# Kernel tuning notes

Measured on AMD Instinct MI355X. Metric: run time of the kernel, lower is better.

## Reference

```python
import jax, jax.numpy as jnp
import numpy as np

B, S, D, E, NH, R, L = 512, 23, 768, 8, 8, 256, 50
TOP_K = 2
LN_EPS = 1e-5  # torch LayerNorm default


def _ln(x, g, b):
    m = jnp.mean(x, axis=-1, keepdims=True)
    v = jnp.mean((x - m) ** 2, axis=-1, keepdims=True)
    return (x - m) * jax.lax.rsqrt(v + LN_EPS) * g + b


def setup_inputs() -> dict:
    key = jax.random.key(0)
    it = iter(jax.random.split(key, 32))
    def p(shape, scale=0.02):
        return jax.random.normal(next(it), shape, dtype=jnp.float32) * scale
    inp = {
        'section_embeddings': jax.random.normal(next(it), (B, S, D), dtype=jnp.float32),
        'existing': jax.random.randint(next(it), (B, S), 0, 2, dtype=jnp.int32),
        'missing_table': p((S, D), 0.05),
        # DeepPositionEncoder per expert (num_layers=3): D->R->R->R->D + LN(D)
        'dpe_w0': p((E, D, R)), 'dpe_b0': jnp.zeros((E, R), jnp.float32),
        'dpe_w1': p((E, R, R)), 'dpe_b1': jnp.zeros((E, R), jnp.float32),
        'dpe_w2': p((E, R, R)), 'dpe_b2': jnp.zeros((E, R), jnp.float32),
        'dpe_wo': p((E, R, D)), 'dpe_bo': jnp.zeros((E, D), jnp.float32),
        'dpe_ln_g': jnp.ones((E, D), jnp.float32), 'dpe_ln_b': jnp.zeros((E, D), jnp.float32),
        # fusion_mlp: cat([context,pos]) (2D)->R->D ; W1 split into context/pos halves
        'fus_w1c': p((E, D, R)), 'fus_w1p': p((E, D, R)), 'fus_b1': jnp.zeros((E, R), jnp.float32),
        'fus_w2': p((E, R, D)), 'fus_b2': jnp.zeros((E, D), jnp.float32),
        # gate_mlp: 2D->R->1, sigmoid
        'gate_w1c': p((E, D, R)), 'gate_w1p': p((E, D, R)), 'gate_b1': jnp.zeros((E, R), jnp.float32),
        'gate_w2': p((E, R, 1)), 'gate_b2': jnp.zeros((E, 1), jnp.float32),
        'exp_ln_g': jnp.ones((E, D), jnp.float32), 'exp_ln_b': jnp.zeros((E, D), jnp.float32),
        # router: 2D->R->E
        'rtr_w1': p((2 * D, R)), 'rtr_b1': jnp.zeros((R,), jnp.float32),
        'rtr_w2': p((R, E)), 'rtr_b2': jnp.zeros((E,), jnp.float32),
        # SectionDimReducer: D->D//2->R + LN(R)
        'red_w1': p((D, D // 2)), 'red_b1': jnp.zeros((D // 2,), jnp.float32),
        'red_w2': p((D // 2, R)), 'red_b2': jnp.zeros((R,), jnp.float32),
        'red_ln_g': jnp.ones((R,), jnp.float32), 'red_ln_b': jnp.zeros((R,), jnp.float32),
        # MultiheadAttention (embed_dim=R, heads=NH)
        'qkv_w': p((3, R, R)), 'qkv_b': jnp.zeros((3, R), jnp.float32),
        'out_w': p((R, R)), 'out_b': jnp.zeros((R,), jnp.float32),
        # predictor
        'pred_w': p((R, L)), 'pred_b': jnp.zeros((L,), jnp.float32),
    }
    return inp


def reference(section_embeddings, existing, missing_table,
              dpe_w0, dpe_b0, dpe_w1, dpe_b1, dpe_w2, dpe_b2, dpe_wo, dpe_bo,
              dpe_ln_g, dpe_ln_b,
              fus_w1c, fus_w1p, fus_b1, fus_w2, fus_b2,
              gate_w1c, gate_w1p, gate_b1, gate_w2, gate_b2,
              exp_ln_g, exp_ln_b,
              rtr_w1, rtr_b1, rtr_w2, rtr_b2,
              red_w1, red_b1, red_w2, red_b2, red_ln_g, red_ln_b,
              qkv_w, qkv_b, out_w, out_b, pred_w, pred_b):
    mask = existing.astype(section_embeddings.dtype)[..., None]         # [B,S,1]
    # masked mean context over present sections
    context = (section_embeddings * mask).sum(1) / (mask.sum(1) + 1e-8)  # [B,D]
    T = B * S
    default = jnp.broadcast_to(missing_table[None], (B, S, D)).reshape(T, D)
    ctx = jnp.broadcast_to(context[:, None, :], (B, S, D)).reshape(T, D)
    # --- all experts, dense (as in source) ---
    h = jax.nn.relu(jnp.einsum('td,edh->teh', default, dpe_w0) + dpe_b0)
    h = jax.nn.relu(jnp.einsum('teh,ehk->tek', h, dpe_w1) + dpe_b1)
    h = jax.nn.relu(jnp.einsum('teh,ehk->tek', h, dpe_w2) + dpe_b2)
    pos = _ln(jnp.einsum('teh,ehd->ted', h, dpe_wo) + dpe_bo + default[:, None, :],
              dpe_ln_g, dpe_ln_b)                                        # [T,E,D]
    hf = jax.nn.relu(jnp.einsum('td,edh->teh', ctx, fus_w1c)
                     + jnp.einsum('ted,edh->teh', pos, fus_w1p) + fus_b1)
    cand = jnp.einsum('teh,ehd->ted', hf, fus_w2) + fus_b2
    hg = jax.nn.relu(jnp.einsum('td,edh->teh', ctx, gate_w1c)
                     + jnp.einsum('ted,edh->teh', pos, gate_w1p) + gate_b1)
    gate = jax.nn.sigmoid(jnp.einsum('teh,eho->teo', hg, gate_w2) + gate_b2)  # [T,E,1]
    exp_out = _ln(gate * cand + (1.0 - gate) * ctx[:, None, :], exp_ln_g, exp_ln_b)  # [T,E,D]
    # --- router: softmax -> top-k -> sparse scatter ---
    rin = jnp.concatenate([default, ctx], axis=-1)                      # [T,2D]
    scores = jax.nn.relu(rin @ rtr_w1 + rtr_b1) @ rtr_w2 + rtr_b2       # [T,E]
    w = jax.nn.softmax(scores, axis=-1)
    tv, ti = jax.lax.top_k(w, TOP_K)
    sw = jnp.zeros_like(w).at[jnp.arange(T)[:, None], ti].set(tv)       # [T,E]
    imputed = jnp.einsum('ted,te->td', exp_out, sw).reshape(B, S, D)
    sec = mask * section_embeddings + (1.0 - mask) * imputed            # [B,S,D]
    # --- reducer ---
    x = jax.nn.gelu(sec @ red_w1 + red_b1, approximate=False)
    x = jax.nn.gelu(x @ red_w2 + red_b2, approximate=False)
    x = _ln(x, red_ln_g, red_ln_b)                                      # [B,S,R]
    # --- MHA self-attention over sections ---
    hd = R // NH
    q = (x @ qkv_w[0] + qkv_b[0]).reshape(B, S, NH, hd)
    k = (x @ qkv_w[1] + qkv_b[1]).reshape(B, S, NH, hd)
    v = (x @ qkv_w[2] + qkv_b[2]).reshape(B, S, NH, hd)
    att = jax.nn.softmax(jnp.einsum('bqhd,bkhd->bhqk', q, k) / np.sqrt(hd), axis=-1)
    o = jnp.einsum('bhqk,bkhd->bqhd', att, v).reshape(B, S, R)
    o = o @ out_w + out_b
    logits = o.mean(axis=1) @ pred_w + pred_b                           # [B,L]
    return logits
```

## Files before the change

### kernel.cpp

```cpp
#include <hip/hip_runtime.h>
#include <hip/hip_bf16.h>
#include <math.h>

#define BB  512
#define SS  23
#define DD  768
#define EE  8
#define NHH 8
#define RR  256
#define HDD 32
#define LL  50
#define HH2 384
#define TT  (BB*SS)
#define LN_EPS 1e-5f
#define MAXWORK 1536
#define NCTX 4352
#define NACAP 12288
#define CPAD 64

typedef short v8s __attribute__((ext_vector_type(8)));
typedef float v4f __attribute__((ext_vector_type(4)));

__device__ __forceinline__ float gelu(float v){
  return 0.5f*v*(1.f + erff(v*0.70710678118654752f));
}
__device__ __forceinline__ unsigned short f2b(float v){
  __hip_bfloat16 h = __float2bfloat16(v);
  return *reinterpret_cast<unsigned short*>(&h);
}

__device__ __forceinline__ float block_sum(float v, float* red, int nw){
  #pragma unroll
  for (int o = 32; o > 0; o >>= 1) v += __shfl_down(v, o, 64);
  int wid = threadIdx.x >> 6;
  __syncthreads();
  if ((threadIdx.x & 63) == 0) red[wid] = v;
  __syncthreads();
  float s = 0.f;
  for (int i = 0; i < nw; ++i) s += red[i];
  return s;
}

__global__ void k_context(const float* __restrict__ emb, const int* __restrict__ existing,
                          float* __restrict__ ctx, unsigned short* __restrict__ ctxbf){
  int b = blockIdx.x, tid = threadIdx.x;
  float acc0=0.f, acc1=0.f, acc2=0.f;
  int cnt = 0;
  for (int s = 0; s < SS; ++s){
    if (existing[b*SS + s]){
      ++cnt;
      const float* row = emb + ((size_t)(b*SS + s))*DD;
      acc0 += row[tid]; acc1 += row[tid+256]; acc2 += row[tid+512];
    }
  }
  float inv = 1.0f / ((float)cnt + 1e-8f);
  float v0 = acc0*inv, v1 = acc1*inv, v2 = acc2*inv;
  ctx[(size_t)b*DD + tid      ] = v0;
  ctx[(size_t)b*DD + tid + 256] = v1;
  ctx[(size_t)b*DD + tid + 512] = v2;
  ctxbf[(size_t)b*DD + tid      ] = f2b(v0);
  ctxbf[(size_t)b*DD + tid + 256] = f2b(v1);
  ctxbf[(size_t)b*DD + tid + 512] = f2b(v2);
}

__global__ void k_mtpad(const float* __restrict__ mt, unsigned short* __restrict__ mtbf){
  int row = blockIdx.x, tid = threadIdx.x;
  #pragma unroll
  for (int j = 0; j < 3; ++j){
    int d = tid + j*256;
    float v = (row < SS) ? mt[(size_t)row*DD + d] : 0.f;
    mtbf[(size_t)row*DD + d] = f2b(v);
  }
}

__global__ __launch_bounds__(256) void k_pack(
    const float* __restrict__ red_w1, const float* __restrict__ qkv_w,
    const float* __restrict__ out_w,  const float* __restrict__ fus_w1c,
    const float* __restrict__ gate_w1c, const float* __restrict__ fus_w2,
    const float* __restrict__ rtr_w1,
    const float* __restrict__ dpe_w0, const float* __restrict__ dpe_w1,
    const float* __restrict__ dpe_w2, const float* __restrict__ dpe_wo,
    const float* __restrict__ fus_w1p, const float* __restrict__ gate_w1p,
    const float* __restrict__ red_w2,
    unsigned short* __restrict__ Wr1t, unsigned short* __restrict__ Wqt,
    unsigned short* __restrict__ Wot,  unsigned short* __restrict__ Wct,
    unsigned short* __restrict__ Wf2t,
    unsigned short* __restrict__ W0t,  unsigned short* __restrict__ W1t,
    unsigned short* __restrict__ W2t,  unsigned short* __restrict__ Wot2,
    unsigned short* __restrict__ Wpgt, unsigned short* __restrict__ Wr1rt,
    unsigned short* __restrict__ Wr2t){
  int t = blockIdx.x, tid = threadIdx.x;
  const float* src; unsigned short* dst;
  int Nsrc, stride, tk, tn;
  if (t < 288){ src = red_w1; dst = Wr1t; Nsrc = 384; stride = 768; tk = t % 24; tn = t / 24; }
  else if (t < 480){
    int u = t - 288, m = u >> 6, v2 = u & 63;
    src = qkv_w + (size_t)m*256*256; dst = Wqt + (size_t)m*256*256;
    Nsrc = 256; stride = 256; tk = v2 & 7; tn = v2 >> 3;
  } else if (t < 544){
    int v2 = t - 480;
    src = out_w; dst = Wot; Nsrc = 256; stride = 256; tk = v2 & 7; tn = v2 >> 3;
  } else if (t < 2080){
    int u = t - 544, e = u / 192, v2 = u % 192;
    src = fus_w1c + (size_t)e*DD*RR; dst = Wct + (size_t)(e*256)*768;
    Nsrc = 256; stride = 768; tk = v2 % 24; tn = v2 / 24;
  } else if (t < 3616){
    int u = t - 2080, e = u / 192, v2 = u % 192;
    src = gate_w1c + (size_t)e*DD*RR; dst = Wct + (size_t)(2048 + e*256)*768;
    Nsrc = 256; stride = 768; tk = v2 % 24; tn = v2 / 24;
  } else if (t < 5152){
    int u = t - 3616, e = u / 192, v2 = u % 192;
    src = fus_w2 + (size_t)e*RR*DD; dst = Wf2t + (size_t)e*768*256;
    Nsrc = 768; stride = 256; tk = v2 & 7; tn = v2 >> 3;
  } else if (t < 5344){
    int u = t - 5152;
    src = rtr_w1 + (size_t)768*256; dst = Wct + (size_t)4096*768;
    Nsrc = 256; stride = 768; tk = u % 24; tn = u / 24;
  } else if (t < 6880){
    int u = t - 5344, e = u / 192, v2 = u % 192;
    src = dpe_w0 + (size_t)e*DD*RR; dst = W0t + (size_t)e*256*768;
    Nsrc = 256; stride = 768; tk = v2 % 24; tn = v2 / 24;
  } else if (t < 7392){
    int u = t - 6880, e = u / 64, v2 = u % 64;
    src = dpe_w1 + (size_t)e*RR*RR; dst = W1t + (size_t)e*256*256;
    Nsrc = 256; stride = 256; tk = v2 & 7; tn = v2 >> 3;
  } else if (t < 7904){
    int u = t - 7392, e = u / 64, v2 = u % 64;
    src = dpe_w2 + (size_t)e*RR*RR; dst = W2t + (size_t)e*256*256;
    Nsrc = 256; stride = 256; tk = v2 & 7; tn = v2 >> 3;
  } else if (t < 9440){
    int u = t - 7904, e = u / 192, v2 = u % 192;
    src = dpe_wo + (size_t)e*RR*DD; dst = Wot2 + (size_t)e*768*256;
    Nsrc = 768; stride = 256; tk = v2 & 7; tn = v2 >> 3;
  } else if (t < 10976){
    int u = t - 9440, e = u / 192, v2 = u % 192;
    src = fus_w1p + (size_t)e*DD*RR; dst = Wpgt + (size_t)e*512*768;
    Nsrc = 256; stride = 768; tk = v2 % 24; tn = v2 / 24;
  } else if (t < 12512){
    int u = t - 10976, e = u / 192, v2 = u % 192;
    src = gate_w1p + (size_t)e*DD*RR; dst = Wpgt + (size_t)e*512*768 + (size_t)256*768;
    Nsrc = 256; stride = 768; tk = v2 % 24; tn = v2 / 24;
  } else if (t < 12704){
    int u = t - 12512;
    src = rtr_w1; dst = Wr1rt;
    Nsrc = 256; stride = 768; tk = u % 24; tn = u / 24;
  } else {
    int u = t - 12704;
    src = red_w2; dst = Wr2t;
    Nsrc = 256; stride = 384; tk = u % 12; tn = u / 12;
  }
  __shared__ float lt[32][33];
  int i0 = tid >> 5, j = tid & 31;
  #pragma unroll
  for (int l = 0; l < 4; ++l){
    int i = i0 + l*8;
    lt[i][j] = src[(size_t)(tk*32 + i)*Nsrc + tn*32 + j];
  }
  __syncthreads();
  #pragma unroll
  for (int l = 0; l < 4; ++l){
    int i = i0 + l*8;
    dst[(size_t)(tn*32 + i)*stride + tk*32 + j] = f2b(lt[j][i]);
  }
}

__global__ __launch_bounds__(256) void k_gemm(
    const unsigned short* __restrict__ A, const unsigned short* __restrict__ Bt,
    const float* __restrict__ bias, float* __restrict__ C,
    int M, int N, int K, int epi){
  int m0 = blockIdx.x * 64, n0 = blockIdx.y * 64;
  int tid = threadIdx.x;
  int w = tid >> 6, lane = tid & 63;
  int fm = lane & 15, q = lane >> 4;
  __shared__ unsigned short As[64*72];
  __shared__ unsigned short Bs[64*72];
  v4f acc[4] = {};
  int sr = tid >> 2, scb = (tid & 3) * 16;
  const unsigned short* Aga = A + (size_t)(m0 + sr)*K + scb;
  const unsigned short* Bga = Bt + (size_t)(n0 + sr)*K + scb;
  unsigned short* Asd = As + sr*72 + scb;
  unsigned short* Bsd = Bs + sr*72 + scb;
  for (int k0 = 0; k0 < K; k0 += 64){
    uint4 a0 = *(const uint4*)(Aga + k0);
    uint4 a1 = *(const uint4*)(Aga + k0 + 8);
    uint4 b0 = *(const uint4*)(Bga + k0);
    uint4 b1 = *(const uint4*)(Bga + k0 + 8);
    __syncthreads();
    *(uint4*)Asd = a0; *(uint4*)(Asd + 8) = a1;
    *(uint4*)Bsd = b0; *(uint4*)(Bsd + 8) = b1;
    __syncthreads();
    const unsigned short* ap = As + (w*16 + fm)*72 + q*8;
    const unsigned short* bp = Bs + fm*72 + q*8;
    #pragma unroll
    for (int kk = 0; kk < 2; ++kk){
      v8s af = *(const v8s*)(ap + kk*32);
      #pragma unroll
      for (int j = 0; j < 4; ++j){
        v8s bf = *(const v8s*)(bp + j*16*72 + kk*32);
        acc[j] = __builtin_amdgcn_mfma_f32_16x16x32_bf16(af, bf, acc[j], 0, 0, 0);
      }
    }
  }
  #pragma unroll
  for (int j = 0; j < 4; ++j){
    int n = n0 + j*16 + fm;
    float bv = bias ? bias[n] : 0.f;
    if (epi == 3){
      unsigned short* Cp = (unsigned short*)C + (size_t)(m0 + w*16 + q*4)*N + n;
      #pragma unroll
      for (int r = 0; r < 4; ++r)
        Cp[(size_t)r*N] = f2b(gelu(acc[j][r] + bv));
    } else {
      float* Cp = C + (size_t)(m0 + w*16 + q*4)*N + n;
      #pragma unroll
      for (int r = 0; r < 4; ++r){
        float v = acc[j][r] + bv;
        if (epi == 2) v = gelu(v);
        Cp[(size_t)r*N] = v;
      }
    }
  }
}

__global__ __launch_bounds__(256) void k_gemmb(
    const unsigned short* __restrict__ A, size_t sA,
    const unsigned short* __restrict__ Bt, size_t sB,
    const float* __restrict__ bias, int sbias,
    void* __restrict__ C, size_t sC,
    int M, int N, int K, int epi){
  int e = blockIdx.z;
  const unsigned short* Ae = A + (size_t)e*sA;
  const unsigned short* Be = Bt + (size_t)e*sB;
  const float* biase = bias ? (bias + (size_t)e*sbias) : (const float*)nullptr;
  int m0 = blockIdx.x * 64, n0 = blockIdx.y * 64;
  int tid = threadIdx.x;
  int w = tid >> 6, lane = tid & 63;
  int fm = lane & 15, q = lane >> 4;
  __shared__ unsigned short As[64*72];
  __shared__ unsigned short Bs[64*72];
  v4f acc[4] = {};
  int sr = tid >> 2, scb = (tid & 3) * 16;
  const unsigned short* Aga = Ae + (size_t)(m0 + sr)*K + scb;
  const unsigned short* Bga = Be + (size_t)(n0 + sr)*K + scb;
  unsigned short* Asd = As + sr*72 + scb;
  unsigned short* Bsd = Bs + sr*72 + scb;
  for (int k0 = 0; k0 < K; k0 += 64){
    uint4 a0 = *(const uint4*)(Aga + k0);
    uint4 a1 = *(const uint4*)(Aga + k0 + 8);
    uint4 b0 = *(const uint4*)(Bga + k0);
    uint4 b1 = *(const uint4*)(Bga + k0 + 8);
    __syncthreads();
    *(uint4*)Asd = a0; *(uint4*)(Asd + 8) = a1;
    *(uint4*)Bsd = b0; *(uint4*)(Bsd + 8) = b1;
    __syncthreads();
    const unsigned short* ap = As + (w*16 + fm)*72 + q*8;
    const unsigned short* bp = Bs + fm*72 + q*8;
    #pragma unroll
    for (int kk = 0; kk < 2; ++kk){
      v8s af = *(const v8s*)(ap + kk*32);
      #pragma unroll
      for (int j = 0; j < 4; ++j){
        v8s bf = *(const v8s*)(bp + j*16*72 + kk*32);
        acc[j] = __builtin_amdgcn_mfma_f32_16x16x32_bf16(af, bf, acc[j], 0, 0, 0);
      }
    }
  }
  #pragma unroll
  for (int j = 0; j < 4; ++j){
    int n = n0 + j*16 + fm;
    float bv = biase ? biase[n] : 0.f;
    #pragma unroll
    for (int r = 0; r < 4; ++r){
      float v = acc[j][r] + bv;
      int m = m0 + w*16 + q*4 + r;
      if (epi == 0){
        unsigned short* Cb = (unsigned short*)C + (size_t)e*sC;
        Cb[(size_t)m*N + n] = f2b(fmaxf(v, 0.f));
      } else {
        float* Cf = (float*)C + (size_t)e*sC;
        Cf[(size_t)m*N + n] = v;
      }
    }
  }
}

__global__ void k_posLN(const float* __restrict__ dpeout, const float* __restrict__ mt,
                        const float* __restrict__ lng, const float* __restrict__ lnb,
                        unsigned short* __restrict__ posbf){
  int e = blockIdx.x >> 6, s = blockIdx.x & 63, tid = threadIdx.x;
  size_t ro = (size_t)(e*64 + s)*DD;
  if (s >= SS){
    for (int j = tid; j < DD; j += 256) posbf[ro + j] = 0;
    return;
  }
  __shared__ float red[8];
  float o[3];
  #pragma unroll
  for (int j = 0; j < 3; ++j){
    int d = tid + j*256;
    o[j] = dpeout[ro + d] + mt[(size_t)s*DD + d];
  }
  float mean = block_sum(o[0]+o[1]+o[2], red, 4) * (1.f/DD);
  float dv = 0.f;
  #pragma unroll
  for (int j = 0; j < 3; ++j){ float c = o[j]-mean; dv += c*c; }
  float rstd = rsqrtf(block_sum(dv, red, 4) * (1.f/DD) + LN_EPS);
  #pragma unroll
  for (int j = 0; j < 3; ++j){
    int d = tid + j*256;
    posbf[ro + d] = f2b((o[j]-mean)*rstd*lng[e*DD + d] + lnb[e*DD + d]);
  }
}

__global__ __launch_bounds__(256) void k_router(
    const float* __restrict__ emb, const int* __restrict__ existing,
    const float* __restrict__ rtrD, const float* __restrict__ ctxFGR,
    const float* __restrict__ rb1, const float* __restrict__ rw2,
    const float* __restrict__ rb2,
    int* __restrict__ cntE, int* __restrict__ listE,
    int* __restrict__ bp0, int* __restrict__ bp1, float* __restrict__ w01,
    unsigned short* __restrict__ secbf){
  int wv = threadIdx.x >> 6, lane = threadIdx.x & 63;
  int tid = threadIdx.x;
  int t = blockIdx.x*4 + wv;
  __shared__ int   easc[8];
  __shared__ int   slotA[8];
  int ex = existing[t];
  if (ex){
    const float4* src = (const float4*)(emb + (size_t)t*DD);
    uint2* dst = (uint2*)(secbf + (size_t)t*DD);
    #pragma unroll
    for (int j = 0; j < 3; ++j){
      float4 x = src[lane + j*64];
      uint2 pk;
      pk.x = (unsigned)f2b(x.x) | ((unsigned)f2b(x.y) << 16);
      pk.y = (unsigned)f2b(x.z) | ((unsigned)f2b(x.w) << 16);
      dst[lane + j*64] = pk;
    }
    if (lane == 0){ easc[2*wv] = -1; easc[2*wv+1] = -1; }
  } else {
    int b = t / SS, s = t - b*SS;
    const float* rtrC = ctxFGR + (size_t)b*NCTX + 4096;
    float acc[EE] = {};
    #pragma unroll
    for (int j = 0; j < 4; ++j){
      int idx = lane + j*64;
      float hr = fmaxf(rtrD[s*RR + idx] + rtrC[idx] + rb1[idx], 0.f);
      #pragma unroll
      for (int e = 0; e < EE; ++e) acc[e] += hr * rw2[idx*EE + e];
    }
    #pragma unroll
    for (int e = 0; e < EE; ++e)
      #pragma unroll
      for (int o = 32; o > 0; o >>= 1) acc[e] += __shfl_xor(acc[e], o, 64);
    if (lane == 0){
      float sc[EE];
      float m = -1e30f;
      #pragma unroll
      for (int e = 0; e < EE; ++e){ sc[e] = acc[e] + rb2[e]; m = fmaxf(m, sc[e]); }
      float w[EE]; float Z = 0.f;
      #pragma unroll
      for (int e = 0; e < EE; ++e){ w[e] = expf(sc[e]-m); Z += w[e]; }
      int i0 = 0;
      for (int e = 1; e < EE; ++e) if (w[e] > w[i0]) i0 = e;
      int i1 = -1;
      for (int e = 0; e < EE; ++e) if (e != i0 && (i1 < 0 || w[e] > w[i1])) i1 = e;
      float iz = 1.f/Z;
      easc[2*wv]   = i0; w01[2*t]   = w[i0]*iz;
      easc[2*wv+1] = i1; w01[2*t+1] = w[i1]*iz;
    }
  }
  __syncthreads();
  if (tid < EE){
    int e = tid, c = 0;
    #pragma unroll
    for (int j = 0; j < 8; ++j) if (easc[j] == e) ++c;
    if (c){
      int base = atomicAdd(&cntE[e*CPAD], c);
      int sl = base;
      #pragma unroll
      for (int j = 0; j < 8; ++j) if (easc[j] == e) slotA[j] = sl++;
    }
  }
  __syncthreads();
  if (tid < 8){
    int j = tid, e = easc[j];
    if (e >= 0){
      int tt = blockIdx.x*4 + (j >> 1);
      int sl = slotA[j];
      if (sl >= TT) sl = TT - 1;
      listE[e*TT + sl] = tt;
      int bp = (e << 16) | sl;
      if (j & 1) bp1[tt] = bp;
      else       bp0[tt] = bp;
    }
  }
}

__global__ void k_offsE(const int* __restrict__ cntE, int* __restrict__ offE,
                        int* __restrict__ workE, int* __restrict__ wtotE){
  if (threadIdx.x == 0){
    int acc = 0, wb = 0;
    for (int e = 0; e < EE; ++e){
      offE[e] = acc;
      int n = cntE[e*CPAD]; if (n > TT) n = TT;
      acc += n;
      int nb = (n + 63) >> 6;
      for (int j = 0; j < nb && wb < MAXWORK; ++j) workE[wb++] = (e << 16) | j;
    }
    wtotE[0] = wb;
  }
}

__global__ __launch_bounds__(256) void k_hfE(
    const float* __restrict__ ctxFGR, const float* __restrict__ posFG,
    const float* __restrict__ fb1,
    const float* __restrict__ gb1, const float* __restrict__ gw2,
    const float* __restrict__ gb2,
    const int* __restrict__ cntE, const int* __restrict__ offE,
    const int* __restrict__ listE,
    const int* __restrict__ workE, const int* __restrict__ wtotE,
    unsigned short* __restrict__ hfg, float* __restrict__ gatesg){
  int wi = blockIdx.x;
  if (wi >= wtotE[0]) return;
  int ent = workE[wi];
  int e = ent >> 16, chunk = ent & 0xffff;
  int n = cntE[e*CPAD]; if (n > TT) n = TT;
  int nt = n - chunk*64; if (nt > 64) nt = 64;
  int base = offE[e] + chunk*64;
  int tid = threadIdx.x, wv = tid >> 6, lane = tid & 63;
  __shared__ int tb[64], ts[64];
  if (tid < 64){
    int ok = tid < nt;
    int t = listE[e*TT + chunk*64 + (ok ? tid : 0)];
    tb[tid] = t/SS; ts[tid] = t - (t/SS)*SS;
  }
  __syncthreads();
  {
    int row = tid >> 2, cb = (tid & 3) * 64;
    if (row < nt){
      int b = tb[row], s = ts[row];
      const float4* cF = (const float4*)(ctxFGR + (size_t)b*NCTX + e*256 + cb);
      const float4* pF = (const float4*)(posFG + ((size_t)(e*64 + s))*512 + cb);
      const float4* bF = (const float4*)(fb1 + (size_t)e*RR + cb);
      uint2* dst = (uint2*)(hfg + (size_t)(base + row)*256 + cb);
      #pragma unroll
      for (int j = 0; j < 16; ++j){
        float4 a = cF[j], p = pF[j], bb = bF[j];
        uint2 pk;
        pk.x = (unsigned)f2b(fmaxf(a.x+p.x+bb.x, 0.f))
             | ((unsigned)f2b(fmaxf(a.y+p.y+bb.y, 0.f)) << 16);
        pk.y = (unsigned)f2b(fmaxf(a.z+p.z+bb.z, 0.f))
             | ((unsigned)f2b(fmaxf(a.w+p.w+bb.w, 0.f)) << 16);
        dst[j] = pk;
      }
    }
  }
  for (int ii = 0; ii < 16; ++ii){
    int row = wv*16 + ii;
    if (row < nt){
      int b = tb[row], s = ts[row];
      float g = 0.f;
      #pragma unroll
      for (int j = 0; j < 4; ++j){
        int idx = lane + j*64;
        float hg = fmaxf(ctxFGR[(size_t)b*NCTX + 2048 + e*256 + idx]
                         + posFG[((size_t)(e*64 + s))*512 + 256 + idx] + gb1[e*RR + idx], 0.f);
        g += hg * gw2[e*RR + idx];
      }
      #pragma unroll
      for (int o = 32; o > 0; o >>= 1) g += __shfl_xor(g, o, 64);
      if (lane == 0) gatesg[base + row] = 1.f/(1.f + expf(-(g + gb2[e])));
    }
  }
}

__global__ __launch_bounds__(256) void k_gemmE(
    const unsigned short* __restrict__ hfg, const unsigned short* __restrict__ Wf2t,
    const float* __restrict__ fb2, const float* __restrict__ ctx,
    const float* __restrict__ gatesg,
    const int* __restrict__ cntE, const int* __restrict__ offE,
    const int* __restrict__ listE,
    const int* __restrict__ workE, const int* __restrict__ wtotE,
    float* __restrict__ cand){
  int wi = blockIdx.x;
  if (wi >= wtotE[0]) return;
  int ent = workE[wi];
  int e = ent >> 16, chunk = ent & 0xffff;
  int n = cntE[e*CPAD]; if (n > TT) n = TT;
  int nt = n - chunk*64; if (nt > 64) nt = 64;
  int base = offE[e] + chunk*64;
  int nc = blockIdx.y;
  int tid = threadIdx.x, w = tid >> 6, lane = tid & 63;
  int fm = lane & 15, q = lane >> 4;
  __shared__ unsigned short As[64*72];
  __shared__ unsigned short Bs[64*72];
  __shared__ float gl[64];
  __shared__ int tbl[64];
  if (tid < 64){
    int ok = tid < nt;
    int t = listE[e*TT + chunk*64 + (ok ? tid : 0)];
    tbl[tid] = t/SS;
    gl[tid] = gatesg[base + (ok ? tid : 0)];
  }
  v4f acc[4] = {};
  int sr = tid >> 2, scb = (tid & 3) * 16;
  const unsigned short* Aga = hfg + (size_t)(base + sr)*256 + scb;
  const unsigned short* Bga = Wf2t + (size_t)e*768*256 + (size_t)(nc*64 + sr)*256 + scb;
  unsigned short* Asd = As + sr*72 + scb;
  unsigned short* Bsd = Bs + sr*72 + scb;
  for (int k0 = 0; k0 < 256; k0 += 64){
    uint4 a0 = *(const uint4*)(Aga + k0);
    uint4 a1 = *(const uint4*)(Aga + k0 + 8);
    uint4 b0 = *(const uint4*)(Bga + k0);
    uint4 b1 = *(const uint4*)(Bga + k0 + 8);
    __syncthreads();
    *(uint4*)Asd = a0; *(uint4*)(Asd + 8) = a1;
    *(uint4*)Bsd = b0; *(uint4*)(Bsd + 8) = b1;
    __syncthreads();
    const unsigned short* ap = As + (w*16 + fm)*72 + q*8;
    const unsigned short* bp = Bs + fm*72 + q*8;
    #pragma unroll
    for (int kk = 0; kk < 2; ++kk){
      v8s af = *(const v8s*)(ap + kk*32);
      #pragma unroll
      for (int j = 0; j < 4; ++j){
        v8s bf = *(const v8s*)(bp + j*16*72 + kk*32);
        acc[j] = __builtin_amdgcn_mfma_f32_16x16x32_bf16(af, bf, acc[j], 0, 0, 0);
      }
    }
  }
  #pragma unroll
  for (int j = 0; j < 4; ++j){
    int d = nc*64 + j*16 + fm;
    float fb2v = fb2[(size_t)e*DD + d];
    #pragma unroll
    for (int r = 0; r < 4; ++r){
      int row = w*16 + q*4 + r;
      if (row < nt){
        float g = gl[row];
        float cv = ctx[(size_t)tbl[row]*DD + d];
        cand[(size_t)(base + row)*DD + d] = g*(acc[j][r] + fb2v) + (1.f - g)*cv;
      }
    }
  }
}

__global__ void k_gather(const int* __restrict__ existing,
                         const int* __restrict__ bp0, const int* __restrict__ bp1,
                         const float* __restrict__ w01, const int* __restrict__ offE,
                         const float* __restrict__ cand,
                         const float* __restrict__ elng, const float* __restrict__ elnb,
                         unsigned short* __restrict__ secbf){
  int wv = threadIdx.x >> 6, lane = threadIdx.x & 63;
  int t = blockIdx.x*4 + wv;
  if (existing[t]) return;
  int b0v = bp0[t], b1v = bp1[t];
  int e0 = b0v >> 16, e1 = b1v >> 16;
  int g0 = offE[e0] + (b0v & 0xffff);
  int g1 = offE[e1] + (b1v & 0xffff);
  if (g0 >= NACAP) g0 = 0;
  if (g1 >= NACAP) g1 = 0;
  float w0 = w01[2*t], w1 = w01[2*t+1];
  float v0[12], v1[12];
  float s0 = 0.f, q0 = 0.f, s1 = 0.f, q1 = 0.f;
  #pragma unroll
  for (int j = 0; j < 12; ++j){
    int d = lane + j*64;
    v0[j] = cand[(size_t)g0*DD + d];
    v1[j] = cand[(size_t)g1*DD + d];
    s0 += v0[j]; q0 += v0[j]*v0[j];
    s1 += v1[j]; q1 += v1[j]*v1[j];
  }
  #pragma unroll
  for (int o = 32; o > 0; o >>= 1){
    s0 += __shfl_xor(s0, o, 64); q0 += __shfl_xor(q0, o, 64);
    s1 += __shfl_xor(s1, o, 64); q1 += __shfl_xor(q1, o, 64);
  }
  float mean0 = s0*(1.f/DD), mean1 = s1*(1.f/DD);
  float rstd0 = rsqrtf(q0*(1.f/DD) - mean0*mean0 + LN_EPS);
  float rstd1 = rsqrtf(q1*(1.f/DD) - mean1*mean1 + LN_EPS);
  #pragma unroll
  for (int j = 0; j < 12; ++j){
    int d = lane + j*64;
    float o0 = (v0[j]-mean0)*rstd0*elng[e0*DD + d] + elnb[e0*DD + d];
    float o1 = (v1[j]-mean1)*rstd1*elng[e1*DD + d] + elnb[e1*DD + d];
    secbf[(size_t)t*DD + d] = f2b(w0*o0 + w1*o1);
  }
}

__global__ void k_lnR(const float* __restrict__ x2f,
                      const float* __restrict__ lng, const float* __restrict__ lnb,
                      unsigned short* __restrict__ xrbf){
  int wv = threadIdx.x >> 6, lane = threadIdx.x & 63;
  int t = blockIdx.x*4 + wv;
  float v[4];
  float s = 0.f, q = 0.f;
  #pragma unroll
  for (int j = 0; j < 4; ++j){
    v[j] = x2f[(size_t)t*RR + lane + j*64];
    s += v[j]; q += v[j]*v[j];
  }
  #pragma unroll
  for (int o = 32; o > 0; o >>= 1){
    s += __shfl_xor(s, o, 64); q += __shfl_xor(q, o, 64);
  }
  float mean = s*(1.f/RR);
  float rstd = rsqrtf(q*(1.f/RR) - mean*mean + LN_EPS);
  #pragma unroll
  for (int j = 0; j < 4; ++j){
    int d = lane + j*64;
    xrbf[(size_t)t*RR + d] = f2b((v[j]-mean)*rstd*lng[d] + lnb[d]);
  }
}

__global__ void k_attn(const float* __restrict__ qcat, unsigned short* __restrict__ attnbf){
  int bh = blockIdx.x, b = bh / NHH, h = bh % NHH, tid = threadIdx.x;
  __shared__ float qs[SS][HDD], ks[SS][HDD], vs[SS][HDD];
  __shared__ float scr[SS][SS+1];
  for (int idx = tid; idx < SS*HDD; idx += 256){
    int s = idx / HDD, d = idx % HDD;
    size_t g = ((size_t)(b*SS + s))*768 + h*HDD + d;
    qs[s][d] = qcat[g]; ks[s][d] = qcat[g + 256]; vs[s][d] = qcat[g + 512];
  }
  __syncthreads();
  const float scale = 0.17677669529663687f;
  for (int idx = tid; idx < SS*SS; idx += 256){
    int qi = idx / SS, ki = idx % SS;
    float a = 0.f;
    #pragma unroll
    for (int d = 0; d < HDD; ++d) a += qs[qi][d]*ks[ki][d];
    scr[qi][ki] = a*scale;
  }
  __syncthreads();
  if (tid < SS){
    float m = -1e30f;
    for (int ki = 0; ki < SS; ++ki) m = fmaxf(m, scr[tid][ki]);
    float Z = 0.f;
    for (int ki = 0; ki < SS; ++ki){ float e2 = expf(scr[tid][ki]-m); scr[tid][ki] = e2; Z += e2; }
    float iz = 1.f/Z;
    for (int ki = 0; ki < SS; ++ki) scr[tid][ki] *= iz;
  }
  __syncthreads();
  for (int idx = tid; idx < SS*HDD; idx += 256){
    int qi = idx / HDD, d = idx % HDD;
    float a = 0.f;
    for (int ki = 0; ki < SS; ++ki) a += scr[qi][ki]*vs[ki][d];
    attnbf[((size_t)(b*SS + qi))*RR + h*HDD + d] = f2b(a);
  }
}

__global__ void k_final(const float* __restrict__ oproj, const float* __restrict__ pw,
                        const float* __restrict__ pb, float* __restrict__ out){
  int b = blockIdx.x, tid = threadIdx.x;
  __shared__ float om[RR];
  float a = 0.f;
  for (int s = 0; s < SS; ++s) a += oproj[((size_t)(b*SS + s))*RR + tid];
  om[tid] = a * (1.f/SS);
  __syncthreads();
  if (tid < LL){
    float acc = pb[tid];
    for (int h = 0; h < RR; ++h) acc += om[h]*pw[h*LL + tid];
    out[b*LL + tid] = acc;
  }
}

extern "C" void kernel_launch(void* const* d_in, const int* in_sizes, int n_in,
                              void* d_out, int out_size, void* d_ws, size_t ws_size,
                              hipStream_t stream){
  (void)in_sizes; (void)n_in; (void)out_size; (void)ws_size;
  const float* emb      = (const float*)d_in[0];
  const int*   existing = (const int*)d_in[1];
  const float* mt       = (const float*)d_in[2];
  const float* dpe_w0   = (const float*)d_in[3];
  const float* dpe_b0   = (const float*)d_in[4];
  const float* dpe_w1   = (const float*)d_in[5];
  const float* dpe_b1   = (const float*)d_in[6];
  const float* dpe_w2   = (const float*)d_in[7];
  const float* dpe_b2   = (const float*)d_in[8];
  const float* dpe_wo   = (const float*)d_in[9];
  const float* dpe_bo   = (const float*)d_in[10];
  const float* dpe_lng  = (const float*)d_in[11];
  const float* dpe_lnb  = (const float*)d_in[12];
  const float* fus_w1c  = (const float*)d_in[13];
  const float* fus_w1p  = (const float*)d_in[14];
  const float* fus_b1   = (const float*)d_in[15];
  const float* fus_w2   = (const float*)d_in[16];
  const float* fus_b2   = (const float*)d_in[17];
  const float* gate_w1c = (const float*)d_in[18];
  const float* gate_w1p = (const float*)d_in[19];
  const float* gate_b1  = (const float*)d_in[20];
  const float* gate_w2  = (const float*)d_in[21];
  const float* gate_b2  = (const float*)d_in[22];
  const float* exp_lng  = (const float*)d_in[23];
  const float* exp_lnb  = (const float*)d_in[24];
  const float* rtr_w1   = (const float*)d_in[25];
  const float* rtr_b1   = (const float*)d_in[26];
  const float* rtr_w2   = (const float*)d_in[27];
  const float* rtr_b2   = (const float*)d_in[28];
  const float* red_w1   = (const float*)d_in[29];
  const float* red_b1   = (const float*)d_in[30];
  const float* red_w2   = (const float*)d_in[31];
  const float* red_b2   = (const float*)d_in[32];
  const float* red_lng  = (const float*)d_in[33];
  const float* red_lnb  = (const float*)d_in[34];
  const float* qkv_w    = (const float*)d_in[35];
  const float* qkv_b    = (const float*)d_in[36];
  const float* out_w    = (const float*)d_in[37];
  const float* out_b    = (const float*)d_in[38];
  const float* pred_w   = (const float*)d_in[39];
  const float* pred_b   = (const float*)d_in[40];
  float* out = (float*)d_out;

  float* wsf = (float*)d_ws;
  size_t off = 0;
  float* ctx    = wsf + off; off += (size_t)BB*DD;
  unsigned short* ctxbf = (unsigned short*)(wsf + off); off += (size_t)BB*DD/2;
  float* ctxFGR = wsf + off; off += (size_t)BB*NCTX;
  int*   cntE   = (int*)(wsf + off); off += EE*CPAD;
  int*   workE  = (int*)(wsf + off); off += MAXWORK;
  int*   wtot   = (int*)(wsf + off); off += 64;
  int*   offE   = wtot + 8;
  float* regA   = wsf + off; off += (size_t)128*TT;
  int*   listE  = (int*)regA;
  int*   bp0    = (int*)regA + (size_t)EE*TT;
  int*   bp1    = (int*)regA + (size_t)(EE+1)*TT;
  float* w01    = regA + (size_t)(EE+2)*TT;
  unsigned short* attnbf = (unsigned short*)regA;
  float* regB   = wsf + off; off += (size_t)TT*DD/2;
  unsigned short* secbf = (unsigned short*)regB;
  float* oprojf = regB;
  float* regC   = wsf + off; off += (size_t)NACAP*DD;
  float* dpeout = regC;
  unsigned short* posbf = (unsigned short*)(regC + 393216);
  unsigned short* h0    = (unsigned short*)(regC + 589824);
  unsigned short* h1    = (unsigned short*)(regC + 655360);
  unsigned short* h2    = (unsigned short*)(regC + 720896);
  float* cand   = regC;
  unsigned short* x1bf = (unsigned short*)regC;
  float* x2f    = regC + 4718592;
  float* qcat   = regC;
  float* regD   = wsf + off; off += (size_t)NACAP*256/2;
  unsigned short* hfg  = (unsigned short*)regD;
  unsigned short* xrbf = (unsigned short*)regD;
  unsigned short* Wr1t = (unsigned short*)(wsf + off); off += (size_t)768*384/2;
  unsigned short* Wqt  = (unsigned short*)(wsf + off); off += (size_t)768*256/2;
  unsigned short* Wot  = (unsigned short*)(wsf + off); off += (size_t)256*256/2;
  unsigned short* Wct  = (unsigned short*)(wsf + off); off += (size_t)NCTX*768/2;
  unsigned short* Wf2t = (unsigned short*)(wsf + off); off += (size_t)EE*768*256/2;
  unsigned short* mtbf = (unsigned short*)(wsf + off); off += (size_t)64*768/2;
  unsigned short* W0t  = (unsigned short*)(wsf + off); off += (size_t)EE*256*768/2;
  unsigned short* W1t  = (unsigned short*)(wsf + off); off += (size_t)EE*256*256/2;
  unsigned short* W2t  = (unsigned short*)(wsf + off); off += (size_t)EE*256*256/2;
  unsigned short* Wot2 = (unsigned short*)(wsf + off); off += (size_t)EE*768*256/2;
  unsigned short* Wpgt = (unsigned short*)(wsf + off); off += (size_t)EE*512*768/2;
  unsigned short* Wr1rt= (unsigned short*)(wsf + off); off += (size_t)256*768/2;
  unsigned short* Wr2t = (unsigned short*)(wsf + off); off += (size_t)256*384/2;
  float* posFG  = wsf + off; off += (size_t)EE*64*512;
  float* rtrDp  = wsf + off; off += (size_t)64*256;
  float* gatesg = wsf + off; off += (size_t)NACAP;

  k_context<<<BB, 256, 0, stream>>>(emb, existing, ctx, ctxbf);
  k_mtpad  <<<64, 256, 0, stream>>>(mt, mtbf);
  k_pack   <<<12800, 256, 0, stream>>>(red_w1, qkv_w, out_w, fus_w1c, gate_w1c, fus_w2,
                                       rtr_w1, dpe_w0, dpe_w1, dpe_w2, dpe_wo,
                                       fus_w1p, gate_w1p, red_w2,
                                       Wr1t, Wqt, Wot, Wct, Wf2t,
                                       W0t, W1t, W2t, Wot2, Wpgt, Wr1rt, Wr2t);
  k_gemmb<<<dim3(1,4,8),  256, 0, stream>>>(mtbf, 0, W0t, (size_t)256*768,
                                            dpe_b0, 256, h0, (size_t)64*256,
                                            64, 256, 768, 0);
  k_gemmb<<<dim3(1,4,8),  256, 0, stream>>>(h0, (size_t)64*256, W1t, (size_t)256*256,
                                            dpe_b1, 256, h1, (size_t)64*256,
                                            64, 256, 256, 0);
  k_gemmb<<<dim3(1,4,8),  256, 0, stream>>>(h1, (size_t)64*256, W2t, (size_t)256*256,
                                            dpe_b2, 256, h2, (size_t)64*256,
                                            64, 256, 256, 0);
  k_gemmb<<<dim3(1,12,8), 256, 0, stream>>>(h2, (size_t)64*256, Wot2, (size_t)768*256,
                                            dpe_bo, 768, dpeout, (size_t)64*768,
                                            64, 768, 256, 1);
  k_posLN<<<512, 256, 0, stream>>>(dpeout, mt, dpe_lng, dpe_lnb, posbf);
  k_gemmb<<<dim3(1,8,8),  256, 0, stream>>>(posbf, (size_t)64*768, Wpgt, (size_t)512*768,
                                            (const float*)nullptr, 0, posFG, (size_t)64*512,
                                            64, 512, 768, 1);
  k_gemmb<<<dim3(1,4,1),  256, 0, stream>>>(mtbf, 0, Wr1rt, 0,
                                            (const float*)nullptr, 0, rtrDp, 0,
                                            64, 256, 768, 1);
  {
    dim3 g(BB/64, NCTX/64);
    k_gemm <<<g, 256, 0, stream>>>(ctxbf, Wct, (const float*)nullptr, ctxFGR,
                                   BB, NCTX, DD, 0);
  }
  hipMemsetAsync(cntE, 0, EE*CPAD*sizeof(int), stream);
  k_router <<<TT/4, 256, 0, stream>>>(emb, existing, rtrDp, ctxFGR, rtr_b1, rtr_w2, rtr_b2,
                                      cntE, listE, bp0, bp1, w01, secbf);
  k_offsE  <<<1, 64, 0, stream>>>(cntE, offE, workE, wtot);
  k_hfE    <<<384, 256, 0, stream>>>(ctxFGR, posFG, fus_b1,
                                     gate_b1, gate_w2, gate_b2,
                                     cntE, offE, listE, workE, wtot, hfg, gatesg);
  k_gemmE  <<<dim3(384,12), 256, 0, stream>>>(hfg, Wf2t, fus_b2, ctx, gatesg,
                                              cntE, offE, listE, workE, wtot, cand);
  k_gather <<<TT/4, 256, 0, stream>>>(existing, bp0, bp1, w01, offE, cand,
                                      exp_lng, exp_lnb, secbf);
  {
    dim3 g(TT/64, HH2/64);
    k_gemm <<<g, 256, 0, stream>>>(secbf, Wr1t, red_b1, (float*)x1bf, TT, HH2, DD, 3);
  }
  {
    dim3 g(TT/64, RR/64);
    k_gemm <<<g, 256, 0, stream>>>(x1bf, Wr2t, red_b2, x2f, TT, RR, HH2, 2);
  }
  k_lnR    <<<TT/4, 256, 0, stream>>>(x2f, red_lng, red_lnb, xrbf);
  {
    dim3 g(TT/64, 768/64);
    k_gemm <<<g, 256, 0, stream>>>(xrbf, Wqt, qkv_b, qcat, TT, 768, RR, 1);
  }
  k_attn   <<<BB*NHH, 256, 0, stream>>>(qcat, attnbf);
  {
    dim3 g(TT/64, RR/64);
    k_gemm <<<g, 256, 0, stream>>>(attnbf, Wot, out_b, oprojf, TT, RR, RR, 1);
  }
  k_final  <<<BB, 256, 0, stream>>>(oprojf, pred_w, pred_b, out);
}
```

Before: 464.6 us.

## Fuse reducer second GEMM with LayerNorm, store expert candidates in bf16, merge setup kernels

Replaces the second reducer GEMM plus separate LayerNorm kernel with one kernel that computes a full 256-wide row tile, applies GELU, and normalizes in registers, avoiding the fp32 x2f round trip. Expert candidate outputs are written as bf16 instead of fp32, halving that intermediate's traffic at some precision cost. The missing-table conversion and the expert counter reset are folded into the context kernel, removing a launch and a memset. The fused GEMM uses only TT/64 blocks with a large shared tile and 16 accumulators, which reduces parallelism and may lower occupancy.

```diff
diff --git a/kernel.cpp b/kernel.cpp
--- a/kernel.cpp
+++ b/kernel.cpp
@@ -28,6 +28,10 @@
   __hip_bfloat16 h = __float2bfloat16(v);
   return *reinterpret_cast<unsigned short*>(&h);
 }
+__device__ __forceinline__ float b2f(unsigned short u){
+  unsigned int x = ((unsigned)u) << 16;
+  return __uint_as_float(x);
+}
 
 __device__ __forceinline__ float block_sum(float v, float* red, int nw){
   #pragma unroll
@@ -42,8 +46,19 @@
 }
 
 __global__ void k_context(const float* __restrict__ emb, const int* __restrict__ existing,
-                          float* __restrict__ ctx, unsigned short* __restrict__ ctxbf){
+                          const float* __restrict__ mt,
+                          float* __restrict__ ctx, unsigned short* __restrict__ ctxbf,
+                          unsigned short* __restrict__ mtbf, int* __restrict__ cntE){
   int b = blockIdx.x, tid = threadIdx.x;
+  if (b == 0 && tid < EE) cntE[tid*CPAD] = 0;
+  if (b < 64){
+    #pragma unroll
+    for (int j = 0; j < 3; ++j){
+      int d = tid + j*256;
+      float v = (b < SS) ? mt[(size_t)b*DD + d] : 0.f;
+      mtbf[(size_t)b*DD + d] = f2b(v);
+    }
+  }
   float acc0=0.f, acc1=0.f, acc2=0.f;
   int cnt = 0;
   for (int s = 0; s < SS; ++s){
@@ -61,16 +76,6 @@
   ctxbf[(size_t)b*DD + tid      ] = f2b(v0);
   ctxbf[(size_t)b*DD + tid + 256] = f2b(v1);
   ctxbf[(size_t)b*DD + tid + 512] = f2b(v2);
-}
-
-__global__ void k_mtpad(const float* __restrict__ mt, unsigned short* __restrict__ mtbf){
-  int row = blockIdx.x, tid = threadIdx.x;
-  #pragma unroll
-  for (int j = 0; j < 3; ++j){
-    int d = tid + j*256;
-    float v = (row < SS) ? mt[(size_t)row*DD + d] : 0.f;
-    mtbf[(size_t)row*DD + d] = f2b(v);
-  }
 }
 
 __global__ __launch_bounds__(256) void k_pack(
@@ -222,6 +227,86 @@
   }
 }
 
+__global__ __launch_bounds__(256) void k_red2f(
+    const unsigned short* __restrict__ x1bf, const unsigned short* __restrict__ Wr2t,
+    const float* __restrict__ b2v, const float* __restrict__ lng,
+    const float* __restrict__ lnb, unsigned short* __restrict__ xrbf){
+  int m0 = blockIdx.x * 64;
+  int tid = threadIdx.x;
+  int w = tid >> 6, lane = tid & 63;
+  int fm = lane & 15, q = lane >> 4;
+  __shared__ unsigned short As[64*72];
+  __shared__ unsigned short Bs[256*72];
+  __shared__ float sBias[256], sG[256], sB[256];
+  sBias[tid] = b2v[tid]; sG[tid] = lng[tid]; sB[tid] = lnb[tid];
+  v4f acc[16] = {};
+  int sr = tid >> 2, scb = (tid & 3) * 16;
+  const unsigned short* Aga = x1bf + (size_t)(m0 + sr)*HH2 + scb;
+  const unsigned short* Bga = Wr2t + (size_t)tid*HH2;
+  unsigned short* Asd = As + sr*72 + scb;
+  unsigned short* Bsd = Bs + tid*72;
+  for (int k0 = 0; k0 < HH2; k0 += 64){
+    uint4 a0 = *(const uint4*)(Aga + k0);
+    uint4 a1 = *(const uint4*)(Aga + k0 + 8);
+    uint4 b0 = *(const uint4*)(Bga + k0);
+    uint4 b1 = *(const uint4*)(Bga + k0 + 8);
+    uint4 b2 = *(const uint4*)(Bga + k0 + 16);
+    uint4 b3 = *(const uint4*)(Bga + k0 + 24);
+    uint4 b4 = *(const uint4*)(Bga + k0 + 32);
+    uint4 b5 = *(const uint4*)(Bga + k0 + 40);
+    uint4 b6 = *(const uint4*)(Bga + k0 + 48);
+    uint4 b7 = *(const uint4*)(Bga + k0 + 56);
+    __syncthreads();
+    *(uint4*)Asd = a0; *(uint4*)(Asd + 8) = a1;
+    *(uint4*)Bsd = b0;        *(uint4*)(Bsd + 8) = b1;
+    *(uint4*)(Bsd + 16) = b2; *(uint4*)(Bsd + 24) = b3;
+    *(uint4*)(Bsd + 32) = b4; *(uint4*)(Bsd + 40) = b5;
+    *(uint4*)(Bsd + 48) = b6; *(uint4*)(Bsd + 56) = b7;
+    __syncthreads();
+    const unsigned short* ap = As + (w*16 + fm)*72 + q*8;
+    const unsigned short* bp = Bs + fm*72 + q*8;
+    #pragma unroll
+    for (int kk = 0; kk < 2; ++kk){
+      v8s af = *(const v8s*)(ap + kk*32);
+      #pragma unroll
+      for (int j = 0; j < 16; ++j){
+        v8s bf = *(const v8s*)(bp + j*16*72 + kk*32);
+        acc[j] = __builtin_amdgcn_mfma_f32_16x16x32_bf16(af, bf, acc[j], 0, 0, 0);
+      }
+    }
+  }
+  float s[4] = {0.f,0.f,0.f,0.f}, sq[4] = {0.f,0.f,0.f,0.f};
+  #pragma unroll
+  for (int j = 0; j < 16; ++j){
+    float bv = sBias[j*16 + fm];
+    #pragma unroll
+    for (int r = 0; r < 4; ++r){
+      float g = gelu(acc[j][r] + bv);
+      acc[j][r] = g;
+      s[r] += g; sq[r] += g*g;
+    }
+  }
+  #pragma unroll
+  for (int o = 1; o < 16; o <<= 1){
+    #pragma unroll
+    for (int r = 0; r < 4; ++r){
+      s[r]  += __shfl_xor(s[r],  o, 64);
+      sq[r] += __shfl_xor(sq[r], o, 64);
+    }
+  }
+  #pragma unroll
+  for (int r = 0; r < 4; ++r){
+    float mean = s[r] * (1.f/RR);
+    float rstd = rsqrtf(sq[r]*(1.f/RR) - mean*mean + LN_EPS);
+    int row = m0 + w*16 + q*4 + r;
+    #pragma unroll
+    for (int j = 0; j < 16; ++j){
+      int n = j*16 + fm;
+      xrbf[(size_t)row*RR + n] = f2b((acc[j][r]-mean)*rstd*sG[n] + sB[n]);
+    }
+  }
+}
+
 __global__ __launch_bounds__(256) void k_gemmb(
     const unsigned short* __restrict__ A, size_t sA,
     const unsigned short* __restrict__ Bt, size_t sB,
@@ -482,7 +567,7 @@
     const int* __restrict__ cntE, const int* __restrict__ offE,
     const int* __restrict__ listE,
     const int* __restrict__ workE, const int* __restrict__ wtotE,
-    float* __restrict__ cand){
+    unsigned short* __restrict__ candbf){
   int wi = blockIdx.x;
   if (wi >= wtotE[0]) return;
   int ent = workE[wi];
@@ -540,7 +625,7 @@
       if (row < nt){
         float g = gl[row];
         float cv = ctx[(size_t)tbl[row]*DD + d];
-        cand[(size_t)(base + row)*DD + d] = g*(acc[j][r] + fb2v) + (1.f - g)*cv;
+        candbf[(size_t)(base + row)*DD + d] = f2b(g*(acc[j][r] + fb2v) + (1.f - g)*cv);
       }
     }
   }
@@ -549,7 +634,7 @@
 __global__ void k_gather(const int* __restrict__ existing,
                          const int* __restrict__ bp0, const int* __restrict__ bp1,
                          const float* __restrict__ w01, const int* __restrict__ offE,
-                         const float* __restrict__ cand,
+                         const unsigned short* __restrict__ candbf,
                          const float* __restrict__ elng, const float* __restrict__ elnb,
                          unsigned short* __restrict__ secbf){
   int wv = threadIdx.x >> 6, lane = threadIdx.x & 63;
@@ -567,8 +652,8 @@
   #pragma unroll
   for (int j = 0; j < 12; ++j){
     int d = lane + j*64;
-    v0[j] = cand[(size_t)g0*DD + d];
-    v1[j] = cand[(size_t)g1*DD + d];
+    v0[j] = b2f(candbf[(size_t)g0*DD + d]);
+    v1[j] = b2f(candbf[(size_t)g1*DD + d]);
     s0 += v0[j]; q0 += v0[j]*v0[j];
     s1 += v1[j]; q1 += v1[j]*v1[j];
   }
@@ -586,31 +671,6 @@
     float o0 = (v0[j]-mean0)*rstd0*elng[e0*DD + d] + elnb[e0*DD + d];
     float o1 = (v1[j]-mean1)*rstd1*elng[e1*DD + d] + elnb[e1*DD + d];
     secbf[(size_t)t*DD + d] = f2b(w0*o0 + w1*o1);
-  }
-}
-
-__global__ void k_lnR(const float* __restrict__ x2f,
-                      const float* __restrict__ lng, const float* __restrict__ lnb,
-                      unsigned short* __restrict__ xrbf){
-  int wv = threadIdx.x >> 6, lane = threadIdx.x & 63;
-  int t = blockIdx.x*4 + wv;
-  float v[4];
-  float s = 0.f, q = 0.f;
-  #pragma unroll
-  for (int j = 0; j < 4; ++j){
-    v[j] = x2f[(size_t)t*RR + lane + j*64];
-    s += v[j]; q += v[j]*v[j];
-  }
-  #pragma unroll
-  for (int o = 32; o > 0; o >>= 1){
-    s += __shfl_xor(s, o, 64); q += __shfl_xor(q, o, 64);
-  }
-  float mean = s*(1.f/RR);
-  float rstd = rsqrtf(q*(1.f/RR) - mean*mean + LN_EPS);
-  #pragma unroll
-  for (int j = 0; j < 4; ++j){
-    int d = lane + j*64;
-    xrbf[(size_t)t*RR + d] = f2b((v[j]-mean)*rstd*lng[d] + lnb[d]);
   }
 }
 
@@ -736,9 +796,8 @@
   unsigned short* h0    = (unsigned short*)(regC + 589824);
   unsigned short* h1    = (unsigned short*)(regC + 655360);
   unsigned short* h2    = (unsigned short*)(regC + 720896);
-  float* cand   = regC;
+  unsigned short* candbf = (unsigned short*)regC;
   unsigned short* x1bf = (unsigned short*)regC;
-  float* x2f    = regC + 4718592;
   float* qcat   = regC;
   float* regD   = wsf + off; off += (size_t)NACAP*256/2;
   unsigned short* hfg  = (unsigned short*)regD;
@@ -760,8 +819,7 @@
   float* rtrDp  = wsf + off; off += (size_t)64*256;
   float* gatesg = wsf + off; off += (size_t)NACAP;
 
-  k_context<<<BB, 256, 0, stream>>>(emb, existing, ctx, ctxbf);
-  k_mtpad  <<<64, 256, 0, stream>>>(mt, mtbf);
+  k_context<<<BB, 256, 0, stream>>>(emb, existing, mt, ctx, ctxbf, mtbf, cntE);
   k_pack   <<<12800, 256, 0, stream>>>(red_w1, qkv_w, out_w, fus_w1c, gate_w1c, fus_w2,
                                        rtr_w1, dpe_w0, dpe_w1, dpe_w2, dpe_wo,
                                        fus_w1p, gate_w1p, red_w2,
@@ -791,7 +849,6 @@
     k_gemm <<<g, 256, 0, stream>>>(ctxbf, Wct, (const float*)nullptr, ctxFGR,
                                    BB, NCTX, DD, 0);
   }
-  hipMemsetAsync(cntE, 0, EE*CPAD*sizeof(int), stream);
   k_router <<<TT/4, 256, 0, stream>>>(emb, existing, rtrDp, ctxFGR, rtr_b1, rtr_w2, rtr_b2,
                                       cntE, listE, bp0, bp1, w01, secbf);
   k_offsE  <<<1, 64, 0, stream>>>(cntE, offE, workE, wtot);
@@ -799,18 +856,14 @@
                                      gate_b1, gate_w2, gate_b2,
                                      cntE, offE, listE, workE, wtot, hfg, gatesg);
   k_gemmE  <<<dim3(384,12), 256, 0, stream>>>(hfg, Wf2t, fus_b2, ctx, gatesg,
-                                              cntE, offE, listE, workE, wtot, cand);
-  k_gather <<<TT/4, 256, 0, stream>>>(existing, bp0, bp1, w01, offE, cand,
+                                              cntE, offE, listE, workE, wtot, candbf);
+  k_gather <<<TT/4, 256, 0, stream>>>(existing, bp0, bp1, w01, offE, candbf,
                                       exp_lng, exp_lnb, secbf);
   {
     dim3 g(TT/64, HH2/64);
     k_gemm <<<g, 256, 0, stream>>>(secbf, Wr1t, red_b1, (float*)x1bf, TT, HH2, DD, 3);
   }
-  {
-    dim3 g(TT/64, RR/64);
-    k_gemm <<<g, 256, 0, stream>>>(x1bf, Wr2t, red_b2, x2f, TT, RR, HH2, 2);
-  }
-  k_lnR    <<<TT/4, 256, 0, stream>>>(x2f, red_lng, red_lnb, xrbf);
+  k_red2f  <<<TT/64, 256, 0, stream>>>(x1bf, Wr2t, red_b2, red_lng, red_lnb, xrbf);
   {
     dim3 g(TT/64, 768/64);
     k_gemm <<<g, 256, 0, stream>>>(xrbf, Wqt, qkv_b, qcat, TT, 768, RR, 1);
```

New measurement: 496.7 us. +6.9%, slower.
